# Kernel tuning notes

Hardware: AMD Instinct MI355X
Metric: run time of the kernel (lower is better)

## Reference

```python
import jax, jax.numpy as jnp
import numpy as np

CAP_FACTOR = 1.25


def _moe_top1(x, wg, w1, b1, w2, b2):
    """Top-1 switch MoE with capacity-based token dropping.
    x: [T, d]; wg: [d, E]; w1: [E, d, f]; b1: [E, f]; w2: [E, f, d]; b2: [E, d].
    """
    T, d = x.shape
    E = wg.shape[1]
    cap = int(CAP_FACTOR * T / E)
    probs = jax.nn.softmax(x @ wg, axis=-1)            # [T, E]
    idx = jnp.argmax(probs, axis=-1)                   # [T] expert assignment
    gate = jnp.max(probs, axis=-1)                     # [T] gate prob
    oh = jax.nn.one_hot(idx, E, dtype=jnp.int32)       # [T, E]
    # position of each token within its expert's buffer
    pos = (jnp.cumsum(oh, axis=0) * oh).sum(-1) - 1    # [T]
    keep = pos < cap                                   # drop tokens over capacity
    pos_w = jnp.where(keep, pos, cap)                  # dropped -> overflow slot
    # dispatch: scatter tokens into per-expert buffers [E, cap+1, d]
    buf = jnp.zeros((E, cap + 1, d), dtype=x.dtype).at[idx, pos_w].set(x)
    buf = buf[:, :cap]                                 # slice off overflow slot
    # grouped expert FFN
    h = jax.nn.relu(jnp.einsum('ecd,edf->ecf', buf, w1) + b1[:, None, :])
    eo = jnp.einsum('ecf,efd->ecd', h, w2) + b2[:, None, :]
    # combine: gather each token's expert output, scale by gate prob, zero dropped
    pos_g = jnp.minimum(pos_w, cap - 1)
    out = eo[idx, pos_g] * (gate * keep.astype(x.dtype))[:, None]
    return out


def setup_inputs():
    key = jax.random.key(0)
    ks = jax.random.split(key, 12)
    B, S, d, dff, E1, E2 = 8, 2048, 1024, 4096, 8, 16
    s = lambda fan: np.float32(1.0 / np.sqrt(fan))
    return dict(
        x=jax.random.normal(ks[0], (B, S, d), jnp.float32),
        y=jax.random.randint(ks[1], (B,), 0, d),
        wg1=jax.random.normal(ks[2], (d, E1), jnp.float32) * s(d),
        w1a=jax.random.normal(ks[3], (E1, d, dff), jnp.float32) * s(d),
        b1a=jnp.zeros((E1, dff), jnp.float32),
        w2a=jax.random.normal(ks[4], (E1, dff, d), jnp.float32) * s(dff),
        b2a=jnp.zeros((E1, d), jnp.float32),
        wg2=jax.random.normal(ks[5], (d, E2), jnp.float32) * s(d),
        w1b=jax.random.normal(ks[6], (E2, d, dff), jnp.float32) * s(d),
        b1b=jnp.zeros((E2, dff), jnp.float32),
        w2b=jax.random.normal(ks[7], (E2, dff, d), jnp.float32) * s(dff),
        b2b=jnp.zeros((E2, d), jnp.float32),
    )


def reference(x, y, wg1, w1a, b1a, w2a, b2a, wg2, w1b, b1b, w2b, b2b):
    B, S, d = x.shape
    xf = x.reshape(B * S, d)
    m1 = _moe_top1(xf, wg1, w1a, b1a, w2a, b2a)        # moe1(x)
    m2 = _moe_top1(m1, wg2, w1b, b1b, w2b, b2b)        # moe2(moe_out)
    resid = x + m2.reshape(B, S, d)                    # residual add
    sent = resid.mean(axis=1)                          # [B, d] mean-pool -> logits
    logp = jax.nn.log_softmax(sent, axis=-1)
    return -logp[jnp.arange(B), y].mean()              # cross-entropy loss
```

## Files before the change

### kernel.cpp

```cpp
#include <hip/hip_runtime.h>
#include <hip/hip_bf16.h>
#include <cstdint>
#include <cstddef>

#define B_    8
#define S_    2048
#define D_    1024
#define DFF_  4096
#define E1_   8
#define E2_   16
#define T_    (B_*S_)
#define CAP1_ 2560
#define CAP2_ 1280
#define EC_   20480

typedef float f32x4 __attribute__((ext_vector_type(4)));

__device__ __forceinline__ unsigned int pk4fp8(float a, float b, float c, float d) {
  int r = __builtin_amdgcn_cvt_pk_fp8_f32(a, b, 0, false);
  r = __builtin_amdgcn_cvt_pk_fp8_f32(c, d, r, true);
  return (unsigned int)r;
}

template<int E>
__global__ __launch_bounds__(256)
void gate_kernel(const float* __restrict__ X, const float* __restrict__ WG,
                 int* __restrict__ idxO, float* __restrict__ gateO) {
  const int lane = threadIdx.x & 63;
  const int wv   = threadIdx.x >> 6;
  const int t    = blockIdx.x * 4 + wv;
  const float* xr = X + (size_t)t * D_;
  float acc[E];
#pragma unroll
  for (int e = 0; e < E; ++e) acc[e] = 0.f;
#pragma unroll
  for (int i = 0; i < 4; ++i) {
    float4 xv = *(const float4*)(xr + i * 256 + lane * 4);
    int kb = i * 256 + lane * 4;
#pragma unroll
    for (int j = 0; j < 4; ++j) {
      float xs = (&xv.x)[j];
      const float* wr = WG + (size_t)(kb + j) * E;
#pragma unroll
      for (int e = 0; e < E; ++e) acc[e] += xs * wr[e];
    }
  }
#pragma unroll
  for (int e = 0; e < E; ++e) {
    float v = acc[e];
#pragma unroll
    for (int s = 32; s >= 1; s >>= 1) v += __shfl_xor(v, s, 64);
    acc[e] = v;
  }
  if (lane == 0) {
    float mx = acc[0]; int mi = 0;
#pragma unroll
    for (int e = 1; e < E; ++e) if (acc[e] > mx) { mx = acc[e]; mi = e; }
    float s = 0.f;
#pragma unroll
    for (int e = 0; e < E; ++e) s += expf(acc[e] - mx);
    idxO[t]  = mi;
    gateO[t] = 1.0f / s;
  }
}

__global__ __launch_bounds__(1024)
void scan_kernel(const int* __restrict__ idx, int E, int cap,
                 int* __restrict__ pos, int* __restrict__ kept) {
  __shared__ int cnt[16][17];
  __shared__ int gbase[16];
  const int tid = threadIdx.x;
  const int w = tid >> 6, lane = tid & 63;
  if (tid < E) gbase[tid] = 0;
  __syncthreads();
  const unsigned long long lt = (lane == 63) ? 0xFFFFFFFFFFFFFFFFull >> 1
                                             : ((1ull << lane) - 1ull);
  for (int it = 0; it < T_ / 1024; ++it) {
    int t = it * 1024 + tid;
    int mi = idx[t];
    int rank = 0;
    for (int e = 0; e < E; ++e) {
      unsigned long long m = __ballot(mi == e);
      if (lane == 0) cnt[w][e] = __popcll(m);
      if (mi == e) rank = __popcll(m & lt);
    }
    __syncthreads();
    int off = 0;
    for (int w2 = 0; w2 < w; ++w2) off += cnt[w2][mi];
    pos[t] = gbase[mi] + off + rank;
    __syncthreads();
    if (tid < E) {
      int tot = 0;
      for (int w2 = 0; w2 < 16; ++w2) tot += cnt[w2][tid];
      gbase[tid] += tot;
    }
    __syncthreads();
  }
  if (tid < E) kept[tid] = min(gbase[tid], cap);
}

__global__ __launch_bounds__(64)
void scatter_kernel(const float* __restrict__ X, const int* __restrict__ idx,
                    const int* __restrict__ pos, int cap,
                    unsigned char* __restrict__ xbuf, int* __restrict__ tokmap,
                    float* __restrict__ mzero) {
  const int t = blockIdx.x;
  const int lane = threadIdx.x;
  const int p = pos[t];
  if (p < cap) {
    const size_t dst = ((size_t)idx[t] * cap + p) * D_;
    const float* xr = X + (size_t)t * D_;
#pragma unroll
    for (int i = 0; i < 4; ++i) {
      float4 v = *(const float4*)(xr + i * 256 + lane * 4);
      *(unsigned int*)(xbuf + dst + i * 256 + lane * 4) = pk4fp8(v.x, v.y, v.z, v.w);
    }
    if (lane == 0) tokmap[(size_t)idx[t] * cap + p] = t;
  } else {
    float4 z = {0.f, 0.f, 0.f, 0.f};
    float* mr = mzero + (size_t)t * D_;
#pragma unroll
    for (int i = 0; i < 4; ++i) *(float4*)(mr + i * 256 + lane * 4) = z;
  }
}

__global__ __launch_bounds__(256)
void wtrans_kernel(const float* __restrict__ src, unsigned char* __restrict__ dst,
                   int K, int N) {
  __shared__ float t[64][65];
  const int tid = threadIdx.x;
  const size_t eo = (size_t)blockIdx.z * K * N;
  const int k0 = blockIdx.y * 64, n0 = blockIdx.x * 64;
  const float* s = src + eo + (size_t)k0 * N + n0;
  unsigned char* d = dst + eo + (size_t)n0 * K + k0;
#pragma unroll
  for (int i = 0; i < 4; ++i) {
    int k = i * 16 + (tid >> 4);
    int n4 = (tid & 15) * 4;
    float4 v = *(const float4*)(s + (size_t)k * N + n4);
    t[k][n4] = v.x; t[k][n4 + 1] = v.y; t[k][n4 + 2] = v.z; t[k][n4 + 3] = v.w;
  }
  __syncthreads();
#pragma unroll
  for (int i = 0; i < 4; ++i) {
    int n = i * 16 + (tid >> 4);
    int k4 = (tid & 15) * 4;
    *(unsigned int*)(d + (size_t)n * K + k4) =
        pk4fp8(t[k4][n], t[k4 + 1][n], t[k4 + 2][n], t[k4 + 3][n]);
  }
}

#define STG(BASEPTR, H, KT, SLOT) do {                                          \
    const unsigned char* _s = (BASEPTR) + (size_t)((H) * 128) * K + (KT) + st_off; \
    __builtin_amdgcn_global_load_lds((const __attribute__((address_space(1))) void*)_s, \
        (__attribute__((address_space(3))) void*)(smem + (SLOT) + dst0), 16, 0, 0);   \
    __builtin_amdgcn_global_load_lds((const __attribute__((address_space(1))) void*)(_s + (size_t)64 * K), \
        (__attribute__((address_space(3))) void*)(smem + (SLOT) + 8192 + dst0), 16, 0, 0); \
  } while (0)

#define RDA(BUF, MH) do { _Pragma("unroll")                                     \
    for (int m_ = 0; m_ < 4; ++m_) {                                            \
      const char* _p = smem + (BUF) * 65536 + aslot + ((MH) * 4 + m_) * 2048 + vaf; \
      _Pragma("unroll") for (int k_ = 0; k_ < 4; ++k_)                          \
        af[m_][k_] = *(const long long*)(_p + (((2 * k_ + c0) ^ swz7) << 4)); } } while (0)

#define RDB01(BUF, DEST) do { _Pragma("unroll")                                 \
    for (int j_ = 0; j_ < 2; ++j_) {                                            \
      const char* _p = smem + (BUF) * 65536 + bslot + j_ * 2048 + vbf;          \
      _Pragma("unroll") for (int k_ = 0; k_ < 4; ++k_)                          \
        DEST[j_][k_] = *(const long long*)(_p + (((2 * k_ + c0) ^ swz7) << 4)); } } while (0)

#define RDB23(BUF) do { _Pragma("unroll")                                       \
    for (int j_ = 0; j_ < 2; ++j_) {                                            \
      const char* _p = smem + (BUF) * 65536 + bslot + (2 + j_) * 2048 + vbf;    \
      _Pragma("unroll") for (int k_ = 0; k_ < 4; ++k_)                          \
        bfb[j_][k_] = *(const long long*)(_p + (((2 * k_ + c0) ^ swz7) << 4)); } } while (0)

#define QUADN0(MH, BA) do {                                                     \
    __builtin_amdgcn_s_setprio(1);                                              \
    _Pragma("unroll") for (int m_ = 0; m_ < 4; ++m_)                            \
    _Pragma("unroll") for (int j_ = 0; j_ < 2; ++j_)                            \
    _Pragma("unroll") for (int k_ = 0; k_ < 4; ++k_)                            \
      acc[(MH) * 4 + m_][j_] = __builtin_amdgcn_mfma_f32_16x16x32_fp8_fp8(      \
          af[m_][k_], BA[j_][k_], acc[(MH) * 4 + m_][j_], 0, 0, 0);             \
    __builtin_amdgcn_s_setprio(0);                                              \
  } while (0)

#define QUADN1(MH) do {                                                         \
    __builtin_amdgcn_s_setprio(1);                                              \
    _Pragma("unroll") for (int m_ = 0; m_ < 4; ++m_)                            \
    _Pragma("unroll") for (int j_ = 0; j_ < 2; ++j_)                            \
    _Pragma("unroll") for (int k_ = 0; k_ < 4; ++k_)                            \
      acc[(MH) * 4 + m_][2 + j_] = __builtin_amdgcn_mfma_f32_16x16x32_fp8_fp8(  \
          af[m_][k_], bfb[j_][k_], acc[(MH) * 4 + m_][2 + j_], 0, 0, 0);        \
    __builtin_amdgcn_s_setprio(0);                                              \
  } while (0)

#define SB0   __builtin_amdgcn_sched_barrier(0)
#define BAR   __builtin_amdgcn_s_barrier()
#define VM6   do { asm volatile("s_waitcnt vmcnt(6)" ::: "memory"); SB0; } while (0)
#define VM8   do { asm volatile("s_waitcnt vmcnt(8)" ::: "memory"); SB0; } while (0)
#define VM0   do { asm volatile("s_waitcnt vmcnt(0)" ::: "memory"); SB0; } while (0)

template<int MODE>
__global__ __launch_bounds__(512, 2)
void moe_gemm(const unsigned char* __restrict__ A,
              const unsigned char* __restrict__ BT,
              const float* __restrict__ bias, int K, int N, int cap, int nbcnt,
              const int* __restrict__ kept,
              unsigned char* __restrict__ Hout, float* __restrict__ Mout,
              const int* __restrict__ tokmap, const float* __restrict__ gate) {
  __shared__ char smem[131072];
  const int tid  = threadIdx.x;
  const int lane = tid & 63;
  const int wv   = tid >> 6;
  const int wr   = wv >> 2;
  const int wc   = wv & 3;

  const int nwg = gridDim.x;
  const int wg  = (blockIdx.x & 7) * (nwg >> 3) + (blockIdx.x >> 3);
  const int per_grp = nbcnt * 4;
  const int grp = wg / per_grp;
  const int rem = wg - grp * per_grp;
  const int mb  = grp * 4 + (rem & 3);
  const int nb  = rem >> 2;

  const int e  = (mb * 256) / cap;
  const int r0 = mb * 256 - e * cap;
  const int kept_e = kept[e];
  if (r0 >= kept_e) return;
  const unsigned char* Ab = A + (size_t)(mb * 256) * K;
  const unsigned char* Bb = BT + ((size_t)e * N + (size_t)nb * 256) * K;

  f32x4 acc[8][4];
#pragma unroll
  for (int m = 0; m < 8; ++m)
#pragma unroll
    for (int n = 0; n < 4; ++n) acc[m][n] = (f32x4){0.f, 0.f, 0.f, 0.f};

  const int scol   = ((tid & 7) ^ ((tid >> 3) & 7)) * 16;
  const size_t st_off = (size_t)(tid >> 3) * K + scol;
  const int dst0   = tid * 16;

  const int r16  = lane & 15;
  const int l34  = lane >> 4;
  const int c0   = l34 >> 1;
  const int swz7 = r16 & 7;
  const int vaf  = r16 * 128 + (l34 & 1) * 8;
  const int vbf  = (wc & 1) * 8192 + vaf;
  const int aslot = wr * 16384;
  const int bslot = 32768 + (wc >> 1) * 16384;
  long long af[4][4], bA0[2][4], bA1[2][4], bfb[2][4];

  STG(Ab, 0, 0, 0);
  STG(Bb, 0, 0, 32768);
  STG(Bb, 1, 0, 49152);
  STG(Ab, 1, 0, 16384);
  STG(Ab, 0, 128, 65536);
  STG(Bb, 0, 128, 98304);
  STG(Bb, 1, 128, 114688);
  STG(Ab, 1, 128, 81920);
  VM8; BAR;
  RDB01(0, bA0);

  const int NT = K >> 7;
  const int NI = K >> 8;
  for (int i = 0; i < NI; ++i) {
    const bool last = (i == NI - 1);
    const bool s2 = (2 * i + 2) < NT;
    const bool s3 = (2 * i + 3) < NT;
    const int kt1 = (2 * i + 1) << 7;
    const int kt2 = (2 * i + 2) << 7;
    const int kt3 = (2 * i + 3) << 7;

    RDA(0, 0);
    if (i > 0) STG(Ab, 1, kt1, 81920);
    BAR; QUADN0(0, bA0); BAR;
    RDB23(0);
    if (s2) STG(Ab, 0, kt2, 0);
    BAR; QUADN1(0); BAR;
    RDA(0, 1);
    if (s2) STG(Bb, 0, kt2, 32768);
    BAR; QUADN1(1); BAR;
    if (s2) STG(Bb, 1, kt2, 49152);
    if (last) { VM0; } else { VM6; }
    RDB01(1, bA1);
    BAR; QUADN0(1, bA0); BAR;
    RDA(1, 0);
    if (s2) STG(Ab, 1, kt2, 16384);
    BAR; QUADN0(0, bA1); BAR;
    RDB23(1);
    if (s3) STG(Ab, 0, kt3, 65536);
    BAR; QUADN1(0); BAR;
    RDA(1, 1);
    if (s3) STG(Bb, 0, kt3, 98304);
    BAR; QUADN1(1); BAR;
    if (s3) STG(Bb, 1, kt3, 114688);
    if (!last) { VM6; RDB01(0, bA0); }
    BAR; QUADN0(1, bA1); BAR;
  }

  const int rg = lane >> 4;
  float bv[4];
#pragma unroll
  for (int n = 0; n < 4; ++n)
    bv[n] = bias[(size_t)e * N + nb * 256 + wc * 64 + n * 16 + r16];

#pragma unroll
  for (int m = 0; m < 8; ++m) {
#pragma unroll
    for (int r = 0; r < 4; ++r) {
      const int lrow = wr * 128 + m * 16 + rg * 4 + r;
      if (MODE == 0) {
        unsigned char* orow = Hout + (size_t)(mb * 256 + lrow) * N + nb * 256;
        unsigned int q = pk4fp8(fmaxf(acc[m][0][r] + bv[0], 0.f),
                                fmaxf(acc[m][1][r] + bv[1], 0.f),
                                fmaxf(acc[m][2][r] + bv[2], 0.f),
                                fmaxf(acc[m][3][r] + bv[3], 0.f));
        orow[wc * 64 +  0 + r16] = (unsigned char)(q & 0xff);
        orow[wc * 64 + 16 + r16] = (unsigned char)((q >> 8) & 0xff);
        orow[wc * 64 + 32 + r16] = (unsigned char)((q >> 16) & 0xff);
        orow[wc * 64 + 48 + r16] = (unsigned char)(q >> 24);
      } else {
        const int lr = r0 + lrow;
        if (lr < kept_e) {
          const int tok = tokmap[mb * 256 + lrow];
          const float gsc = gate[tok];
          float* orow = Mout + (size_t)tok * N + nb * 256;
#pragma unroll
          for (int n = 0; n < 4; ++n)
            orow[wc * 64 + n * 16 + r16] = (acc[m][n][r] + bv[n]) * gsc;
        }
      }
    }
  }
}

__global__ __launch_bounds__(256)
void reduce_kernel(const float* __restrict__ X, const float* __restrict__ M2,
                   float* __restrict__ sent) {
  const int c = blockIdx.x * 256 + threadIdx.x;
  const int b = blockIdx.z;
  const int s0 = blockIdx.y * 128;
  float a = 0.f;
  size_t base = ((size_t)b * S_ + s0) * D_ + c;
  for (int s = 0; s < 128; ++s) a += X[base + (size_t)s * D_] + M2[base + (size_t)s * D_];
  atomicAdd(&sent[b * D_ + c], a * (1.0f / (float)S_));
}

__global__ __launch_bounds__(64)
void loss_kernel(const float* __restrict__ sent, const int* __restrict__ y,
                 float* __restrict__ out) {
  const int lane = threadIdx.x;
  float total = 0.f;
  for (int b = 0; b < B_; ++b) {
    const float* s = sent + b * D_;
    float v[16];
    float mx = -1e30f;
#pragma unroll
    for (int i = 0; i < 16; ++i) { v[i] = s[lane + i * 64]; mx = fmaxf(mx, v[i]); }
#pragma unroll
    for (int sh = 32; sh >= 1; sh >>= 1) mx = fmaxf(mx, __shfl_xor(mx, sh, 64));
    float sm = 0.f;
#pragma unroll
    for (int i = 0; i < 16; ++i) sm += expf(v[i] - mx);
#pragma unroll
    for (int sh = 32; sh >= 1; sh >>= 1) sm += __shfl_xor(sm, sh, 64);
    total += logf(sm) + mx - s[y[b]];
  }
  if (lane == 0) out[0] = total * (1.0f / (float)B_);
}

extern "C" void kernel_launch(void* const* d_in, const int* in_sizes, int n_in,
                              void* d_out, int out_size, void* d_ws, size_t ws_size,
                              hipStream_t stream) {
  const float* x   = (const float*)d_in[0];
  const int*   y   = (const int*)d_in[1];
  const float* wg1 = (const float*)d_in[2];
  const float* w1a = (const float*)d_in[3];
  const float* b1a = (const float*)d_in[4];
  const float* w2a = (const float*)d_in[5];
  const float* b2a = (const float*)d_in[6];
  const float* wg2 = (const float*)d_in[7];
  const float* w1b = (const float*)d_in[8];
  const float* b1b = (const float*)d_in[9];
  const float* w2b = (const float*)d_in[10];
  const float* b2b = (const float*)d_in[11];
  float* out = (float*)d_out;
  (void)in_sizes; (void)n_in; (void)out_size; (void)ws_size;

  char* base = (char*)d_ws;
  size_t o = 0;
  auto alloc = [&](size_t bytes) { size_t r = o; o = (o + bytes + 255) & ~(size_t)255; return r; };
  int*   idx1    = (int*)  (base + alloc((size_t)T_ * 4));
  int*   pos1    = (int*)  (base + alloc((size_t)T_ * 4));
  float* gate1   = (float*)(base + alloc((size_t)T_ * 4));
  int*   idx2    = (int*)  (base + alloc((size_t)T_ * 4));
  int*   pos2    = (int*)  (base + alloc((size_t)T_ * 4));
  float* gate2   = (float*)(base + alloc((size_t)T_ * 4));
  int*   kept1   = (int*)  (base + alloc(64 * 4));
  int*   kept2   = (int*)  (base + alloc(64 * 4));
  int*   tokmap1 = (int*)  (base + alloc((size_t)EC_ * 4));
  int*   tokmap2 = (int*)  (base + alloc((size_t)EC_ * 4));
  float* sent    = (float*)(base + alloc((size_t)B_ * D_ * 4));
  float* m1      = (float*)(base + alloc((size_t)T_ * D_ * 4));
  unsigned char* xbuf = (unsigned char*)(base + alloc((size_t)EC_ * D_));
  unsigned char* h    = (unsigned char*)(base + alloc((size_t)EC_ * DFF_));
  unsigned char* wT   = (unsigned char*)(base + alloc((size_t)E2_ * D_ * DFF_));

  hipMemsetAsync(sent, 0, (size_t)B_ * D_ * 4, stream);

  gate_kernel<E1_><<<T_ / 4, 256, 0, stream>>>(x, wg1, idx1, gate1);
  scan_kernel<<<1, 1024, 0, stream>>>(idx1, E1_, CAP1_, pos1, kept1);
  scatter_kernel<<<T_, 64, 0, stream>>>(x, idx1, pos1, CAP1_, xbuf, tokmap1, m1);
  wtrans_kernel<<<dim3(DFF_ / 64, D_ / 64, E1_), 256, 0, stream>>>(w1a, wT, D_, DFF_);
  moe_gemm<0><<<(DFF_ / 256) * (EC_ / 256), 512, 0, stream>>>(
      xbuf, wT, b1a, D_, DFF_, CAP1_, DFF_ / 256, kept1, h, nullptr, nullptr, nullptr);
  wtrans_kernel<<<dim3(D_ / 64, DFF_ / 64, E1_), 256, 0, stream>>>(w2a, wT, DFF_, D_);
  moe_gemm<1><<<(D_ / 256) * (EC_ / 256), 512, 0, stream>>>(
      h, wT, b2a, DFF_, D_, CAP1_, D_ / 256, kept1, nullptr, m1, tokmap1, gate1);

  gate_kernel<E2_><<<T_ / 4, 256, 0, stream>>>(m1, wg2, idx2, gate2);
  scan_kernel<<<1, 1024, 0, stream>>>(idx2, E2_, CAP2_, pos2, kept2);
  scatter_kernel<<<T_, 64, 0, stream>>>(m1, idx2, pos2, CAP2_, xbuf, tokmap2, m1);
  wtrans_kernel<<<dim3(DFF_ / 64, D_ / 64, E2_), 256, 0, stream>>>(w1b, wT, D_, DFF_);
  moe_gemm<0><<<(DFF_ / 256) * (EC_ / 256), 512, 0, stream>>>(
      xbuf, wT, b1b, D_, DFF_, CAP2_, DFF_ / 256, kept2, h, nullptr, nullptr, nullptr);
  wtrans_kernel<<<dim3(D_ / 64, DFF_ / 64, E2_), 256, 0, stream>>>(w2b, wT, DFF_, D_);
  moe_gemm<1><<<(D_ / 256) * (EC_ / 256), 512, 0, stream>>>(
      h, wT, b2b, DFF_, D_, CAP2_, D_ / 256, kept2, nullptr, m1, tokmap2, gate2);

  reduce_kernel<<<dim3(D_ / 256, S_ / 128, B_), 256, 0, stream>>>(x, m1, sent);
  loss_kernel<<<1, 64, 0, stream>>>(sent, y, out);
}
```

Before: 1.309 ms.

## Fuse next-stage weight fp8 transpose into preceding MoE GEMM launches

Removes three standalone weight-transpose launches. The transpose of each next stage's weights now runs inside the preceding GEMM launch, in 128 extra worker blocks that convert fp32 to fp8 and transpose through shared memory. A second packed-weight buffer is added so the next weights can be written while the current ones are read. This overlaps memory-bound weight conversion with compute-bound GEMM work and cuts launch gaps. The cost is extra workspace, and the worker blocks compete with GEMM blocks for CUs and bandwidth.

Result: faster. 1.246 ms (-4.8%).

```diff
diff --git a/kernel.cpp b/kernel.cpp
--- a/kernel.cpp
+++ b/kernel.cpp
@@ -207,18 +207,48 @@
 void moe_gemm(const unsigned char* __restrict__ A,
               const unsigned char* __restrict__ BT,
               const float* __restrict__ bias, int K, int N, int cap, int nbcnt,
+              int ntl,
               const int* __restrict__ kept,
               unsigned char* __restrict__ Hout, float* __restrict__ Mout,
-              const int* __restrict__ tokmap, const float* __restrict__ gate) {
+              const int* __restrict__ tokmap, const float* __restrict__ gate,
+              const float* __restrict__ tsrc, unsigned char* __restrict__ tdst,
+              int tK, int tN, int tE, int nwrk) {
   __shared__ char smem[131072];
   const int tid  = threadIdx.x;
+
+  if (tsrc != nullptr && (int)blockIdx.x < nwrk) {
+    const int ntn = tN >> 7, ntk = tK >> 7;
+    const int tiles = tE * ntk * ntn;
+    const int krow = tid >> 2;
+    const int kq   = (tid & 3) * 32;
+    for (int t = blockIdx.x; t < tiles; t += nwrk) {
+      const int e2 = t / (ntk * ntn), rm = t - e2 * (ntk * ntn);
+      const int k0 = (rm / ntn) << 7, n0 = (rm - (rm / ntn) * ntn) << 7;
+      const float* s = tsrc + (size_t)e2 * tK * tN + (size_t)(k0 + krow) * tN + n0 + kq;
+#pragma unroll
+      for (int j = 0; j < 8; ++j) {
+        float4 v = *(const float4*)(s + j * 4);
+        unsigned int q = pk4fp8(v.x, v.y, v.z, v.w);
+#pragma unroll
+        for (int b = 0; b < 4; ++b)
+          smem[(kq + j * 4 + b) * 128 + krow] = (char)((q >> (8 * b)) & 0xff);
+      }
+      __syncthreads();
+      unsigned char* d = tdst + (size_t)e2 * tK * tN + (size_t)(n0 + krow) * tK + k0 + kq;
+      *(uint4*)(d)      = *(const uint4*)(smem + krow * 128 + kq);
+      *(uint4*)(d + 16) = *(const uint4*)(smem + krow * 128 + kq + 16);
+      __syncthreads();
+    }
+    return;
+  }
+
+  const int gbid = (int)blockIdx.x - (tsrc ? nwrk : 0);
   const int lane = tid & 63;
   const int wv   = tid >> 6;
   const int wr   = wv >> 2;
   const int wc   = wv & 3;
 
-  const int nwg = gridDim.x;
-  const int wg  = (blockIdx.x & 7) * (nwg >> 3) + (blockIdx.x >> 3);
+  const int wg  = (gbid & 7) * (ntl >> 3) + (gbid >> 3);
   const int per_grp = nbcnt * 4;
   const int grp = wg / per_grp;
   const int rem = wg - grp * per_grp;
@@ -406,29 +436,35 @@
   float* m1      = (float*)(base + alloc((size_t)T_ * D_ * 4));
   unsigned char* xbuf = (unsigned char*)(base + alloc((size_t)EC_ * D_));
   unsigned char* h    = (unsigned char*)(base + alloc((size_t)EC_ * DFF_));
-  unsigned char* wT   = (unsigned char*)(base + alloc((size_t)E2_ * D_ * DFF_));
+  unsigned char* P1   = (unsigned char*)(base + alloc((size_t)E2_ * D_ * DFF_));
+  unsigned char* P2   = (unsigned char*)(base + alloc((size_t)E2_ * D_ * DFF_));
 
   hipMemsetAsync(sent, 0, (size_t)B_ * D_ * 4, stream);
+
+  const int NT0 = (DFF_ / 256) * (EC_ / 256);
+  const int NT1 = (D_  / 256) * (EC_ / 256);
+  const int NW  = 128;
 
   gate_kernel<E1_><<<T_ / 4, 256, 0, stream>>>(x, wg1, idx1, gate1);
   scan_kernel<<<1, 1024, 0, stream>>>(idx1, E1_, CAP1_, pos1, kept1);
   scatter_kernel<<<T_, 64, 0, stream>>>(x, idx1, pos1, CAP1_, xbuf, tokmap1, m1);
-  wtrans_kernel<<<dim3(DFF_ / 64, D_ / 64, E1_), 256, 0, stream>>>(w1a, wT, D_, DFF_);
-  moe_gemm<0><<<(DFF_ / 256) * (EC_ / 256), 512, 0, stream>>>(
-      xbuf, wT, b1a, D_, DFF_, CAP1_, DFF_ / 256, kept1, h, nullptr, nullptr, nullptr);
-  wtrans_kernel<<<dim3(D_ / 64, DFF_ / 64, E1_), 256, 0, stream>>>(w2a, wT, DFF_, D_);
-  moe_gemm<1><<<(D_ / 256) * (EC_ / 256), 512, 0, stream>>>(
-      h, wT, b2a, DFF_, D_, CAP1_, D_ / 256, kept1, nullptr, m1, tokmap1, gate1);
+  wtrans_kernel<<<dim3(DFF_ / 64, D_ / 64, E1_), 256, 0, stream>>>(w1a, P1, D_, DFF_);
+  moe_gemm<0><<<NT0 + NW, 512, 0, stream>>>(
+      xbuf, P1, b1a, D_, DFF_, CAP1_, DFF_ / 256, NT0, kept1, h, nullptr, nullptr, nullptr,
+      w2a, P2, DFF_, D_, E1_, NW);
+  moe_gemm<1><<<NT1 + NW, 512, 0, stream>>>(
+      h, P2, b2a, DFF_, D_, CAP1_, D_ / 256, NT1, kept1, nullptr, m1, tokmap1, gate1,
+      w1b, P1, D_, DFF_, E2_, NW);
 
   gate_kernel<E2_><<<T_ / 4, 256, 0, stream>>>(m1, wg2, idx2, gate2);
   scan_kernel<<<1, 1024, 0, stream>>>(idx2, E2_, CAP2_, pos2, kept2);
   scatter_kernel<<<T_, 64, 0, stream>>>(m1, idx2, pos2, CAP2_, xbuf, tokmap2, m1);
-  wtrans_kernel<<<dim3(DFF_ / 64, D_ / 64, E2_), 256, 0, stream>>>(w1b, wT, D_, DFF_);
-  moe_gemm<0><<<(DFF_ / 256) * (EC_ / 256), 512, 0, stream>>>(
-      xbuf, wT, b1b, D_, DFF_, CAP2_, DFF_ / 256, kept2, h, nullptr, nullptr, nullptr);
-  wtrans_kernel<<<dim3(D_ / 64, DFF_ / 64, E2_), 256, 0, stream>>>(w2b, wT, DFF_, D_);
-  moe_gemm<1><<<(D_ / 256) * (EC_ / 256), 512, 0, stream>>>(
-      h, wT, b2b, DFF_, D_, CAP2_, D_ / 256, kept2, nullptr, m1, tokmap2, gate2);
+  moe_gemm<0><<<NT0 + NW, 512, 0, stream>>>(
+      xbuf, P1, b1b, D_, DFF_, CAP2_, DFF_ / 256, NT0, kept2, h, nullptr, nullptr, nullptr,
+      w2b, P2, DFF_, D_, E2_, NW);
+  moe_gemm<1><<<NT1, 512, 0, stream>>>(
+      h, P2, b2b, DFF_, D_, CAP2_, D_ / 256, NT1, kept2, nullptr, m1, tokmap2, gate2,
+      nullptr, nullptr, 0, 0, 0, 0);
 
   reduce_kernel<<<dim3(D_ / 256, S_ / 128, B_), 256, 0, stream>>>(x, m1, sent);
   loss_kernel<<<1, 64, 0, stream>>>(sent, y, out);
```
